# Optimization experiments

Hardware: AMD Instinct MI355X
Metric: run time of the kernel (lower is better)

The kernel has to match this reference:

```python
import jax, jax.numpy as jnp
import numpy as np

# Fixed query graph: 3 terms, 3 predicates, edges (head_term, tail_term, pred):
# (0,1,0), (1,2,1), (0,2,2) -> every term has degree 2 -> seq_len 3 incl. self.
T, P, B, D, H, NL, FF = 3, 3, 16384, 256, 8, 2, 1024
DH = D // H
SCALE = DH ** -0.5


def setup_inputs() -> dict:
    key = jax.random.key(0)
    ks = jax.random.split(key, 8)
    s = 0.02
    f = jnp.float32
    return {
        "term_embs": jax.random.normal(ks[0], (T, B, D), f),
        "pred_embs": jax.random.normal(ks[1], (P, B, D), f),
        "Wq": jax.random.normal(ks[2], (NL, D, D), f) * s,
        "Wk": jax.random.normal(ks[3], (NL, D, D), f) * s,
        "Wv": jax.random.normal(ks[4], (NL, D, D), f) * s,
        "Wo": jax.random.normal(ks[5], (NL, D, D), f) * s,
        "bq": jnp.zeros((NL, D), f),
        "bk": jnp.zeros((NL, D), f),
        "bv": jnp.zeros((NL, D), f),
        "bo": jnp.zeros((NL, D), f),
        "ln1_g": jnp.ones((NL, D), f),
        "ln1_b": jnp.zeros((NL, D), f),
        "ln2_g": jnp.ones((NL, D), f),
        "ln2_b": jnp.zeros((NL, D), f),
        "W1": jax.random.normal(ks[6], (NL, D, FF), f) * s,
        "b1": jnp.zeros((NL, FF), f),
        "W2": jax.random.normal(ks[7], (NL, FF, D), f) * s,
        "b2": jnp.zeros((NL, D), f),
        "lnf_g": jnp.ones((D,), f),
        "lnf_b": jnp.zeros((D,), f),
    }


def _layer_norm(x, g, b):
    m = jnp.mean(x, axis=-1, keepdims=True)
    v = jnp.var(x, axis=-1, keepdims=True)
    return (x - m) * jax.lax.rsqrt(v + 1e-5) * g + b


def _forward(term_embs, pred_embs, Wq, Wk, Wv, Wo, bq, bk, bv, bo,
             ln1_g, ln1_b, ln2_g, ln2_b, W1, b1, W2, b2, lnf_g, lnf_b):
    # --- message passing (TransE-style NBP): tail_est = head + pred, head_est = tail - pred
    # edge heads: [0,1,0], edge tails: [1,2,2]
    tail_msgs = term_embs[jnp.array([0, 1, 0])] + pred_embs  # [P,B,D] -> sent to tail terms
    head_msgs = term_embs[jnp.array([1, 2, 2])] - pred_embs  # [P,B,D] -> sent to head terms
    # collect per term (static gather) + self embedding appended last
    x0 = jnp.stack([head_msgs[0], head_msgs[2], term_embs[0]], axis=1)  # [B,3,D]
    x1 = jnp.stack([tail_msgs[0], head_msgs[1], term_embs[1]], axis=1)
    x2 = jnp.stack([tail_msgs[1], tail_msgs[2], term_embs[2]], axis=1)
    x = jnp.concatenate([x0, x1, x2], axis=0)  # [T*B, 3, D]
    # --- pre-norm Transformer encoder, NL layers (dropout off at eval)
    for l in range(NL):
        h = _layer_norm(x, ln1_g[l], ln1_b[l])
        q = (h @ Wq[l] + bq[l]).reshape(-1, 3, H, DH)
        k = (h @ Wk[l] + bk[l]).reshape(-1, 3, H, DH)
        v = (h @ Wv[l] + bv[l]).reshape(-1, 3, H, DH)
        a = jax.nn.softmax(jnp.einsum('nqhd,nkhd->nhqk', q, k) * SCALE, axis=-1)
        o = jnp.einsum('nhqk,nkhd->nqhd', a, v).reshape(-1, 3, D)
        x = x + o @ Wo[l] + bo[l]
        h = _layer_norm(x, ln2_g[l], ln2_b[l])
        x = x + jax.nn.relu(h @ W1[l] + b1[l]) @ W2[l] + b2[l]
    x = _layer_norm(x, lnf_g, lnf_b)
    # --- aggregate (agg_func='mean') over the small message sequence
    return jnp.mean(x, axis=1).reshape(T, B, D)


def reference(term_embs, pred_embs, Wq, Wk, Wv, Wo, bq, bk, bv, bo,
              ln1_g, ln1_b, ln2_g, ln2_b, W1, b1, W2, b2, lnf_g, lnf_b):
    return _forward(term_embs, pred_embs, Wq, Wk, Wv, Wo, bq, bk, bv, bo,
                    ln1_g, ln1_b, ln2_g, ln2_b, W1, b1, W2, b2, lnf_g, lnf_b)
```

## Files before the change

kernel.cpp:

```cpp
#include <hip/hip_runtime.h>
#include <hip/hip_bf16.h>
#include <stdint.h>

typedef __hip_bfloat16 bf16;
typedef unsigned short u16;
typedef unsigned int u32;
typedef __bf16 v8bf __attribute__((ext_vector_type(8)));
typedef float v4f __attribute__((ext_vector_type(4)));

#define NB 16384
#define MROWS 147456

__device__ __forceinline__ float b2f(u16 u) {
  union { u32 u; float f; } v; v.u = ((u32)u) << 16; return v.f;
}
__device__ __forceinline__ u16 f2b(float f) {
  union { float f; u32 u; } v; v.f = f;
  u32 u = v.u;
  return (u16)((u + 0x7fffu + ((u >> 16) & 1u)) >> 16);
}
__device__ __forceinline__ void async16(const u16* g, u16* lds) {
  __builtin_amdgcn_global_load_lds((const __attribute__((address_space(1))) void*)g,
                                   (__attribute__((address_space(3))) void*)lds,
                                   16, 0, 0);
}

__global__ __launch_bounds__(256)
void prep_weights(const float* Wq, const float* Wk, const float* Wv, const float* Wo,
                  const float* W1, const float* W2,
                  const float* bq, const float* bk, const float* bv,
                  bf16* wt, float* bqkv)
{
  if (blockIdx.x == 6144) {
    for (int e = threadIdx.x; e < 1536; e += 256) {
      int l = e / 768;
      int rem = e - l * 768;
      int wsel = rem >> 8;
      int col = rem & 255;
      const float* s = (wsel == 0) ? bq : (wsel == 1) ? bk : bv;
      bqkv[e] = s[l * 256 + col];
    }
    return;
  }
  int gid = blockIdx.x * 256 + threadIdx.x;
  int layer = (gid >= 786432) ? 1 : 0;
  int r = gid - layer * 786432;
  const float* src; int K, N, e, outoff;
  if (r < 262144) {
    int which = r >> 16;
    e = r & 65535; K = 256; N = 256;
    const float* w = (which == 0) ? Wq : (which == 1) ? Wk : (which == 2) ? Wv : Wo;
    src = w + layer * 65536;
    outoff = layer * 786432 + which * 65536;
  } else if (r < 524288) {
    e = r - 262144; K = 256; N = 1024;
    src = W1 + layer * 262144;
    outoff = layer * 786432 + 262144;
  } else {
    e = r - 524288; K = 1024; N = 256;
    src = W2 + layer * 262144;
    outoff = layer * 786432 + 524288;
  }
  int n = e / K, kk = e - n * K;
  ((u16*)wt)[outoff + e] = f2b(src[kk * N + n]);
}

__global__ __launch_bounds__(256)
void build_ln(const float* __restrict__ T, const float* __restrict__ P,
              const float* __restrict__ gp, const float* __restrict__ bp,
              float* __restrict__ X, bf16* __restrict__ H, int row0)
{
  const int lane = threadIdx.x & 63;
  const int lrow = blockIdx.x * 4 + (threadIdx.x >> 6);
  const int row = row0 + lrow;
  const int d0 = lane * 4;
  int n = row / 3;
  int t = row - n * 3;
  float4 v;
  if (t == 2) {
    v = *(const float4*)(T + (size_t)n * 256 + d0);
  } else {
    int tm = n >> 14, b = n & 16383;
    const int srcT[6] = {1, 2,  0, 2,  1, 0};
    const int srcP[6] = {0, 2,  0, 1,  1, 2};
    const float sg[6] = {-1.f, -1.f,  1.f, -1.f,  1.f, 1.f};
    int idx = tm * 2 + t;
    float4 tv = *(const float4*)(T + ((size_t)(srcT[idx] * NB + b)) * 256 + d0);
    float4 pv = *(const float4*)(P + ((size_t)(srcP[idx] * NB + b)) * 256 + d0);
    float s = sg[idx];
    v.x = tv.x + s * pv.x;
    v.y = tv.y + s * pv.y;
    v.z = tv.z + s * pv.z;
    v.w = tv.w + s * pv.w;
  }
  *(float4*)(X + (size_t)lrow * 256 + d0) = v;
  float s = v.x + v.y + v.z + v.w;
  float q = v.x * v.x + v.y * v.y + v.z * v.z + v.w * v.w;
  #pragma unroll
  for (int m = 32; m > 0; m >>= 1) {
    s += __shfl_xor(s, m, 64);
    q += __shfl_xor(q, m, 64);
  }
  float mean = s * (1.f / 256.f);
  float var = q * (1.f / 256.f) - mean * mean;
  float r = rsqrtf(var + 1e-5f);
  float4 gv = *(const float4*)(gp + d0);
  float4 bv = *(const float4*)(bp + d0);
  ushort4 outv;
  outv.x = f2b((v.x - mean) * r * gv.x + bv.x);
  outv.y = f2b((v.y - mean) * r * gv.y + bv.y);
  outv.z = f2b((v.z - mean) * r * gv.z + bv.z);
  outv.w = f2b((v.w - mean) * r * gv.w + bv.w);
  *(ushort4*)((u16*)H + (size_t)lrow * 256 + d0) = outv;
}

__global__ __launch_bounds__(256)
void ln_rows(const float* __restrict__ xp, const float* __restrict__ gp,
             const float* __restrict__ bp, bf16* __restrict__ hp)
{
  const int lane = threadIdx.x & 63;
  const int row = blockIdx.x * 4 + (threadIdx.x >> 6);
  float4 rv = *(const float4*)(xp + (size_t)row * 256 + lane * 4);
  float v0 = rv.x, v1 = rv.y, v2 = rv.z, v3 = rv.w;
  float s = v0 + v1 + v2 + v3;
  float q = v0 * v0 + v1 * v1 + v2 * v2 + v3 * v3;
  #pragma unroll
  for (int m = 32; m > 0; m >>= 1) {
    s += __shfl_xor(s, m, 64);
    q += __shfl_xor(q, m, 64);
  }
  float mean = s * (1.f / 256.f);
  float var = q * (1.f / 256.f) - mean * mean;
  float r = rsqrtf(var + 1e-5f);
  float4 gv = *(const float4*)(gp + lane * 4);
  float4 bv = *(const float4*)(bp + lane * 4);
  ushort4 outv;
  outv.x = f2b((v0 - mean) * r * gv.x + bv.x);
  outv.y = f2b((v1 - mean) * r * gv.y + bv.y);
  outv.z = f2b((v2 - mean) * r * gv.z + bv.z);
  outv.w = f2b((v3 - mean) * r * gv.w + bv.w);
  *(ushort4*)((u16*)hp + (size_t)row * 256 + lane * 4) = outv;
}

template<int RES, int RELU, int OUTF32>
__global__ __launch_bounds__(256)
void gemm_bt(const bf16* __restrict__ Ap, const bf16* __restrict__ Btp,
             const float* __restrict__ biasp, const float* __restrict__ resp,
             void* __restrict__ Cp, int N, int K,
             int btZ, int biasZ, long long cZ)
{
  __shared__ __align__(16) u16 As[2 * 128 * 32];
  __shared__ __align__(16) u16 Bs[2 * 128 * 32];
  const int z = blockIdx.z;
  const u16* A = (const u16*)Ap;
  const u16* Bt = (const u16*)Btp + (size_t)z * btZ;
  const float* bias = biasp + (size_t)z * biasZ;
  const int m0 = blockIdx.x * 128;
  const int n0 = blockIdx.y * 128;
  const int tid = threadIdx.x;
  const int w = tid >> 6, lane = tid & 63;
  const int waveM = (w & 1) * 64, waveN = (w >> 1) * 64;

  const int rrow = tid >> 2;
  const int kcol = (tid & 3) * 8;
  const u16* pA0 = A + (size_t)(m0 + rrow) * K + kcol;
  const u16* pA1 = A + (size_t)(m0 + rrow + 64) * K + kcol;
  const u16* pB0 = Bt + (size_t)(n0 + rrow) * K + kcol;
  const u16* pB1 = Bt + (size_t)(n0 + rrow + 64) * K + kcol;

  v4f acc[4][4];
  #pragma unroll
  for (int i = 0; i < 4; i++)
    #pragma unroll
    for (int j = 0; j < 4; j++) {
      v4f zz = {0.f, 0.f, 0.f, 0.f};
      acc[i][j] = zz;
    }

  const int rdA = (waveM + (lane & 15)) * 64 + (lane >> 4) * 16;
  const int rdB = (waveN + (lane & 15)) * 64 + (lane >> 4) * 16;
  const int nk = K >> 5;

  async16(pA0, As + w * 512);        async16(pA1, As + 2048 + w * 512);
  async16(pB0, Bs + w * 512);        async16(pB1, Bs + 2048 + w * 512);
  pA0 += 32; pA1 += 32; pB0 += 32; pB1 += 32;

  int cur = 0;
  for (int kt = 0; kt < nk; kt++) {
    __syncthreads();
    if (kt + 1 < nk) {
      const int nxt = (cur ^ 1) * 4096;
      async16(pA0, As + nxt + w * 512);        async16(pA1, As + nxt + 2048 + w * 512);
      async16(pB0, Bs + nxt + w * 512);        async16(pB1, Bs + nxt + 2048 + w * 512);
      pA0 += 32; pA1 += 32; pB0 += 32; pB1 += 32;
    }
    const char* AsC = (const char*)(As + cur * 4096);
    const char* BsC = (const char*)(Bs + cur * 4096);
    v8bf a[4], b[4];
    #pragma unroll
    for (int i = 0; i < 4; i++)
      a[i] = *(const v8bf*)(AsC + rdA + i * 1024);
    #pragma unroll
    for (int j = 0; j < 4; j++)
      b[j] = *(const v8bf*)(BsC + rdB + j * 1024);
    #pragma unroll
    for (int i = 0; i < 4; i++)
      #pragma unroll
      for (int j = 0; j < 4; j++)
        acc[i][j] = __builtin_amdgcn_mfma_f32_16x16x32_bf16(a[i], b[j], acc[i][j], 0, 0, 0);
    cur ^= 1;
  }

  float bv[4];
  #pragma unroll
  for (int j = 0; j < 4; j++)
    bv[j] = bias[n0 + waveN + j * 16 + (lane & 15)];

  #pragma unroll
  for (int i = 0; i < 4; i++) {
    #pragma unroll
    for (int r = 0; r < 4; r++) {
      int rowg = m0 + waveM + i * 16 + (lane >> 4) * 4 + r;
      size_t rb = (size_t)rowg * N;
      #pragma unroll
      for (int j = 0; j < 4; j++) {
        int colg = n0 + waveN + j * 16 + (lane & 15);
        float vv = acc[i][j][r] + bv[j];
        if (RES) vv += resp[rb + colg];
        if (RELU) vv = fmaxf(vv, 0.f);
        if (OUTF32) ((float*)Cp)[rb + colg] = vv;
        else ((u16*)Cp + (size_t)z * cZ)[rb + colg] = f2b(vv);
      }
    }
  }
}

__global__ __launch_bounds__(256)
void attn(const bf16* __restrict__ qp, const bf16* __restrict__ kp,
          const bf16* __restrict__ vp, bf16* __restrict__ op)
{
  __shared__ __align__(16) u16 qs[6144], ks[6144], vs[6144];
  __shared__ float probs[8][8][9];
  const int tid = threadIdx.x;
  const size_t gbase = (size_t)blockIdx.x * 6144;
  const uint4* qg = (const uint4*)((const u16*)qp + gbase);
  const uint4* kg = (const uint4*)((const u16*)kp + gbase);
  const uint4* vg = (const uint4*)((const u16*)vp + gbase);
  for (int c = tid; c < 768; c += 256) {
    ((uint4*)qs)[c] = qg[c];
    ((uint4*)ks)[c] = kg[c];
    ((uint4*)vs)[c] = vg[c];
  }
  __syncthreads();
  if (tid < 64) {
    int s = tid >> 3, h = tid & 7;
    int base = s * 768 + h * 32;
    float sc[3][3];
    #pragma unroll
    for (int i = 0; i < 3; i++)
      #pragma unroll
      for (int j = 0; j < 3; j++) {
        float sum = 0.f;
        #pragma unroll
        for (int d = 0; d < 32; d++)
          sum += b2f(qs[base + i * 256 + d]) * b2f(ks[base + j * 256 + d]);
        sc[i][j] = sum * 0.17677669529663687f;
      }
    #pragma unroll
    for (int i = 0; i < 3; i++) {
      float m = fmaxf(sc[i][0], fmaxf(sc[i][1], sc[i][2]));
      float e0 = __expf(sc[i][0] - m);
      float e1 = __expf(sc[i][1] - m);
      float e2 = __expf(sc[i][2] - m);
      float inv = 1.f / (e0 + e1 + e2);
      probs[s][h][i * 3 + 0] = e0 * inv;
      probs[s][h][i * 3 + 1] = e1 * inv;
      probs[s][h][i * 3 + 2] = e2 * inv;
    }
  }
  __syncthreads();
  u16* og = (u16*)op + gbase;
  for (int c = tid; c < 6144; c += 256) {
    int lrow = c >> 8, hd = c & 255;
    int s = lrow / 3, i = lrow - s * 3;
    int h = hd >> 5;
    float p0 = probs[s][h][i * 3 + 0];
    float p1 = probs[s][h][i * 3 + 1];
    float p2 = probs[s][h][i * 3 + 2];
    float o = p0 * b2f(vs[s * 768 + hd])
            + p1 * b2f(vs[s * 768 + 256 + hd])
            + p2 * b2f(vs[s * 768 + 512 + hd]);
    og[c] = f2b(o);
  }
}

__global__ __launch_bounds__(256)
void ln_final_mean(const float* __restrict__ xp, const float* __restrict__ gp,
                   const float* __restrict__ bp, float* __restrict__ outp)
{
  const int lane = threadIdx.x & 63;
  const int n = blockIdx.x * 4 + (threadIdx.x >> 6);
  float4 gv = *(const float4*)(gp + lane * 4);
  float4 bv4 = *(const float4*)(bp + lane * 4);
  float a0 = 0.f, a1 = 0.f, a2 = 0.f, a3 = 0.f;
  for (int t = 0; t < 3; t++) {
    float4 rv = *(const float4*)(xp + ((size_t)n * 3 + t) * 256 + lane * 4);
    float v0 = rv.x, v1 = rv.y, v2 = rv.z, v3 = rv.w;
    float s = v0 + v1 + v2 + v3;
    float q = v0 * v0 + v1 * v1 + v2 * v2 + v3 * v3;
    #pragma unroll
    for (int m = 32; m > 0; m >>= 1) {
      s += __shfl_xor(s, m, 64);
      q += __shfl_xor(q, m, 64);
    }
    float mean = s * (1.f / 256.f);
    float var = q * (1.f / 256.f) - mean * mean;
    float r = rsqrtf(var + 1e-5f);
    a0 += (v0 - mean) * r * gv.x + bv4.x;
    a1 += (v1 - mean) * r * gv.y + bv4.y;
    a2 += (v2 - mean) * r * gv.z + bv4.z;
    a3 += (v3 - mean) * r * gv.w + bv4.w;
  }
  const float third = 1.f / 3.f;
  float4 outv;
  outv.x = a0 * third;
  outv.y = a1 * third;
  outv.z = a2 * third;
  outv.w = a3 * third;
  *(float4*)(outp + (size_t)n * 256 + lane * 4) = outv;
}

extern "C" void kernel_launch(void* const* d_in, const int* in_sizes, int n_in,
                              void* d_out, int out_size, void* d_ws, size_t ws_size,
                              hipStream_t stream)
{
  const float* term = (const float*)d_in[0];
  const float* pred = (const float*)d_in[1];
  const float* Wq  = (const float*)d_in[2];
  const float* Wk  = (const float*)d_in[3];
  const float* Wv  = (const float*)d_in[4];
  const float* Wo  = (const float*)d_in[5];
  const float* bq  = (const float*)d_in[6];
  const float* bk  = (const float*)d_in[7];
  const float* bvv = (const float*)d_in[8];
  const float* bo  = (const float*)d_in[9];
  const float* ln1g = (const float*)d_in[10];
  const float* ln1b = (const float*)d_in[11];
  const float* ln2g = (const float*)d_in[12];
  const float* ln2b = (const float*)d_in[13];
  const float* W1  = (const float*)d_in[14];
  const float* b1  = (const float*)d_in[15];
  const float* W2  = (const float*)d_in[16];
  const float* b2  = (const float*)d_in[17];
  const float* lnfg = (const float*)d_in[18];
  const float* lnfb = (const float*)d_in[19];

  int nch = 128;
  for (int c = 1; c <= 128; c *= 2) {
    size_t Mc = (size_t)MROWS / c;
    size_t need = 4ull * 1024 * 1024 + Mc * 3584ull;
    if (need <= ws_size) { nch = c; break; }
  }
  const size_t Mc = (size_t)MROWS / nch;
  const int mBlocks = (int)(Mc / 128);

  char* ws = (char*)d_ws;
  bf16* wt   = (bf16*)ws;
  float* bqkv = (float*)(ws + 3145728);
  float* x = (float*)(ws + 4194304);
  bf16* h = (bf16*)(x + Mc * 256);
  bf16* q = h + Mc * 256;
  bf16* v_ = q + 2 * Mc * 256;
  bf16* o = q + 3 * Mc * 256;
  bf16* f = q;

  prep_weights<<<6145, 256, 0, stream>>>(Wq, Wk, Wv, Wo, W1, W2, bq, bk, bvv, wt, bqkv);

  const long long qkvZ = (long long)(Mc * 256);
  for (int ch = 0; ch < nch; ch++) {
    const int row0 = (int)(ch * Mc);
    build_ln<<<(int)(Mc / 4), 256, 0, stream>>>(term, pred, ln1g, ln1b, x, h, row0);
    for (int l = 0; l < 2; l++) {
      const bf16* wl = wt + l * 786432;
      if (l > 0)
        ln_rows<<<(int)(Mc / 4), 256, 0, stream>>>(x, ln1g + l * 256, ln1b + l * 256, h);
      gemm_bt<0, 0, 0><<<dim3(mBlocks, 2, 3), 256, 0, stream>>>(
          h, wl, bqkv + l * 768, nullptr, q, 256, 256, 65536, 256, qkvZ);
      attn<<<(int)(Mc / 24), 256, 0, stream>>>(q, q + Mc * 256, v_, o);
      gemm_bt<1, 0, 1><<<dim3(mBlocks, 2, 1), 256, 0, stream>>>(
          o, wl + 196608, bo + l * 256, x, x, 256, 256, 0, 0, 0);
      ln_rows<<<(int)(Mc / 4), 256, 0, stream>>>(x, ln2g + l * 256, ln2b + l * 256, h);
      gemm_bt<0, 1, 0><<<dim3(mBlocks, 8, 1), 256, 0, stream>>>(
          h, wl + 262144, b1 + l * 1024, nullptr, f, 1024, 256, 0, 0, 0);
      gemm_bt<1, 0, 1><<<dim3(mBlocks, 2, 1), 256, 0, stream>>>(
          f, wl + 524288, b2 + l * 256, x, x, 256, 1024, 0, 0, 0);
    }
    ln_final_mean<<<(int)(Mc / 12), 256, 0, stream>>>(
        x, lnfg, lnfb, (float*)d_out + (size_t)(row0 / 3) * 256);
  }
}
```

Before: 1.592 ms.

## Register-prefetch GEMM pipeline and fuse QKV into one interleaved GEMM output

The GEMM drops the global_load_lds async copies. It now stages tiles through registers with a two-deep prefetch: it loads tiles kt+3 and kt+4 into registers while computing on LDS double buffers, unrolled by two. The Q, K and V projections become a single N=768 GEMM writing an interleaved row layout, and the attention kernel reads strided q/k/v slices from it. This is meant to hide global latency better and remove the z-dimension indexing. The cost is more register pressure, and the layout relies on the weights being packed contiguously as a 768x256 block.

```diff
diff --git a/kernel.cpp b/kernel.cpp
--- a/kernel.cpp
+++ b/kernel.cpp
@@ -18,11 +18,6 @@
   union { float f; u32 u; } v; v.f = f;
   u32 u = v.u;
   return (u16)((u + 0x7fffu + ((u >> 16) & 1u)) >> 16);
-}
-__device__ __forceinline__ void async16(const u16* g, u16* lds) {
-  __builtin_amdgcn_global_load_lds((const __attribute__((address_space(1))) void*)g,
-                                   (__attribute__((address_space(3))) void*)lds,
-                                   16, 0, 0);
 }
 
 __global__ __launch_bounds__(256)
@@ -142,19 +137,49 @@
   *(ushort4*)((u16*)hp + (size_t)row * 256 + lane * 4) = outv;
 }
 
+#define LDT(dst, t) do {                                            \
+    int tt = (t) < nk ? (t) : nk - 1;                               \
+    dst[0] = *(const uint4*)(pA0 + tt * 32);                        \
+    dst[1] = *(const uint4*)(pA1 + tt * 32);                        \
+    dst[2] = *(const uint4*)(pB0 + tt * 32);                        \
+    dst[3] = *(const uint4*)(pB1 + tt * 32);                        \
+  } while (0)
+
+#define WRT(src, buf) do {                                          \
+    ((uint4*)As)[(buf) * 512 + tid] = src[0];                       \
+    ((uint4*)As)[(buf) * 512 + 256 + tid] = src[1];                 \
+    ((uint4*)Bs)[(buf) * 512 + tid] = src[2];                       \
+    ((uint4*)Bs)[(buf) * 512 + 256 + tid] = src[3];                 \
+  } while (0)
+
+#define CMPT(buf) do {                                              \
+    const char* AsC = (const char*)As + (buf) * 8192;               \
+    const char* BsC = (const char*)Bs + (buf) * 8192;               \
+    v8bf a[4], b[4];                                                \
+    _Pragma("unroll")                                               \
+    for (int i = 0; i < 4; i++)                                     \
+      a[i] = *(const v8bf*)(AsC + rdA + i * 1024);                  \
+    _Pragma("unroll")                                               \
+    for (int j = 0; j < 4; j++)                                     \
+      b[j] = *(const v8bf*)(BsC + rdB + j * 1024);                  \
+    _Pragma("unroll")                                               \
+    for (int i = 0; i < 4; i++)                                     \
+      _Pragma("unroll")                                             \
+      for (int j = 0; j < 4; j++)                                   \
+        acc[i][j] = __builtin_amdgcn_mfma_f32_16x16x32_bf16(        \
+            a[i], b[j], acc[i][j], 0, 0, 0);                        \
+  } while (0)
+
 template<int RES, int RELU, int OUTF32>
 __global__ __launch_bounds__(256)
 void gemm_bt(const bf16* __restrict__ Ap, const bf16* __restrict__ Btp,
              const float* __restrict__ biasp, const float* __restrict__ resp,
-             void* __restrict__ Cp, int N, int K,
-             int btZ, int biasZ, long long cZ)
+             void* __restrict__ Cp, int N, int K)
 {
   __shared__ __align__(16) u16 As[2 * 128 * 32];
   __shared__ __align__(16) u16 Bs[2 * 128 * 32];
-  const int z = blockIdx.z;
   const u16* A = (const u16*)Ap;
-  const u16* Bt = (const u16*)Btp + (size_t)z * btZ;
-  const float* bias = biasp + (size_t)z * biasZ;
+  const u16* Bt = (const u16*)Btp;
   const int m0 = blockIdx.x * 128;
   const int n0 = blockIdx.y * 128;
   const int tid = threadIdx.x;
@@ -164,9 +189,10 @@
   const int rrow = tid >> 2;
   const int kcol = (tid & 3) * 8;
   const u16* pA0 = A + (size_t)(m0 + rrow) * K + kcol;
-  const u16* pA1 = A + (size_t)(m0 + rrow + 64) * K + kcol;
+  const u16* pA1 = pA0 + (size_t)64 * K;
   const u16* pB0 = Bt + (size_t)(n0 + rrow) * K + kcol;
-  const u16* pB1 = Bt + (size_t)(n0 + rrow + 64) * K + kcol;
+  const u16* pB1 = pB0 + (size_t)64 * K;
+  const int nk = K >> 5;
 
   v4f acc[4][4];
   #pragma unroll
@@ -179,42 +205,29 @@
 
   const int rdA = (waveM + (lane & 15)) * 64 + (lane >> 4) * 16;
   const int rdB = (waveN + (lane & 15)) * 64 + (lane >> 4) * 16;
-  const int nk = K >> 5;
-
-  async16(pA0, As + w * 512);        async16(pA1, As + 2048 + w * 512);
-  async16(pB0, Bs + w * 512);        async16(pB1, Bs + 2048 + w * 512);
-  pA0 += 32; pA1 += 32; pB0 += 32; pB1 += 32;
-
-  int cur = 0;
-  for (int kt = 0; kt < nk; kt++) {
+
+  uint4 R[4], S[4];
+  LDT(R, 0);
+  LDT(S, 1);
+  WRT(R, 0);
+  LDT(R, 2);
+  __syncthreads();
+
+  for (int kt = 0; kt < nk; kt += 2) {
+    WRT(S, 1);
+    LDT(S, kt + 3);
+    CMPT(0);
     __syncthreads();
-    if (kt + 1 < nk) {
-      const int nxt = (cur ^ 1) * 4096;
-      async16(pA0, As + nxt + w * 512);        async16(pA1, As + nxt + 2048 + w * 512);
-      async16(pB0, Bs + nxt + w * 512);        async16(pB1, Bs + nxt + 2048 + w * 512);
-      pA0 += 32; pA1 += 32; pB0 += 32; pB1 += 32;
-    }
-    const char* AsC = (const char*)(As + cur * 4096);
-    const char* BsC = (const char*)(Bs + cur * 4096);
-    v8bf a[4], b[4];
-    #pragma unroll
-    for (int i = 0; i < 4; i++)
-      a[i] = *(const v8bf*)(AsC + rdA + i * 1024);
-    #pragma unroll
-    for (int j = 0; j < 4; j++)
-      b[j] = *(const v8bf*)(BsC + rdB + j * 1024);
-    #pragma unroll
-    for (int i = 0; i < 4; i++)
-      #pragma unroll
-      for (int j = 0; j < 4; j++)
-        acc[i][j] = __builtin_amdgcn_mfma_f32_16x16x32_bf16(a[i], b[j], acc[i][j], 0, 0, 0);
-    cur ^= 1;
+    WRT(R, 0);
+    LDT(R, kt + 4);
+    CMPT(1);
+    __syncthreads();
   }
 
   float bv[4];
   #pragma unroll
   for (int j = 0; j < 4; j++)
-    bv[j] = bias[n0 + waveN + j * 16 + (lane & 15)];
+    bv[j] = biasp[n0 + waveN + j * 16 + (lane & 15)];
 
   #pragma unroll
   for (int i = 0; i < 4; i++) {
@@ -229,27 +242,24 @@
         if (RES) vv += resp[rb + colg];
         if (RELU) vv = fmaxf(vv, 0.f);
         if (OUTF32) ((float*)Cp)[rb + colg] = vv;
-        else ((u16*)Cp + (size_t)z * cZ)[rb + colg] = f2b(vv);
+        else ((u16*)Cp)[rb + colg] = f2b(vv);
       }
     }
   }
 }
 
 __global__ __launch_bounds__(256)
-void attn(const bf16* __restrict__ qp, const bf16* __restrict__ kp,
-          const bf16* __restrict__ vp, bf16* __restrict__ op)
+void attn(const bf16* __restrict__ qkvp, bf16* __restrict__ op)
 {
   __shared__ __align__(16) u16 qs[6144], ks[6144], vs[6144];
   __shared__ float probs[8][8][9];
   const int tid = threadIdx.x;
-  const size_t gbase = (size_t)blockIdx.x * 6144;
-  const uint4* qg = (const uint4*)((const u16*)qp + gbase);
-  const uint4* kg = (const uint4*)((const u16*)kp + gbase);
-  const uint4* vg = (const uint4*)((const u16*)vp + gbase);
+  const uint4* g = (const uint4*)qkvp + (size_t)blockIdx.x * 24 * 96;
   for (int c = tid; c < 768; c += 256) {
-    ((uint4*)qs)[c] = qg[c];
-    ((uint4*)ks)[c] = kg[c];
-    ((uint4*)vs)[c] = vg[c];
+    int r = c >> 5, e = c & 31;
+    ((uint4*)qs)[c] = g[r * 96 + e];
+    ((uint4*)ks)[c] = g[r * 96 + 32 + e];
+    ((uint4*)vs)[c] = g[r * 96 + 64 + e];
   }
   __syncthreads();
   if (tid < 64) {
@@ -279,7 +289,7 @@
     }
   }
   __syncthreads();
-  u16* og = (u16*)op + gbase;
+  u16* og = (u16*)op + (size_t)blockIdx.x * 6144;
   for (int c = tid; c < 6144; c += 256) {
     int lrow = c >> 8, hd = c & 255;
     int s = lrow / 3, i = lrow - s * 3;
@@ -369,14 +379,12 @@
   float* bqkv = (float*)(ws + 3145728);
   float* x = (float*)(ws + 4194304);
   bf16* h = (bf16*)(x + Mc * 256);
-  bf16* q = h + Mc * 256;
-  bf16* v_ = q + 2 * Mc * 256;
-  bf16* o = q + 3 * Mc * 256;
-  bf16* f = q;
+  bf16* qkv = h + Mc * 256;
+  bf16* o = qkv + Mc * 768;
+  bf16* f = qkv;
 
   prep_weights<<<6145, 256, 0, stream>>>(Wq, Wk, Wv, Wo, W1, W2, bq, bk, bvv, wt, bqkv);
 
-  const long long qkvZ = (long long)(Mc * 256);
   for (int ch = 0; ch < nch; ch++) {
     const int row0 = (int)(ch * Mc);
     build_ln<<<(int)(Mc / 4), 256, 0, stream>>>(term, pred, ln1g, ln1b, x, h, row0);
@@ -384,16 +392,16 @@
       const bf16* wl = wt + l * 786432;
       if (l > 0)
         ln_rows<<<(int)(Mc / 4), 256, 0, stream>>>(x, ln1g + l * 256, ln1b + l * 256, h);
-      gemm_bt<0, 0, 0><<<dim3(mBlocks, 2, 3), 256, 0, stream>>>(
-          h, wl, bqkv + l * 768, nullptr, q, 256, 256, 65536, 256, qkvZ);
-      attn<<<(int)(Mc / 24), 256, 0, stream>>>(q, q + Mc * 256, v_, o);
-      gemm_bt<1, 0, 1><<<dim3(mBlocks, 2, 1), 256, 0, stream>>>(
-          o, wl + 196608, bo + l * 256, x, x, 256, 256, 0, 0, 0);
+      gemm_bt<0, 0, 0><<<dim3(mBlocks, 6), 256, 0, stream>>>(
+          h, wl, bqkv + l * 768, nullptr, qkv, 768, 256);
+      attn<<<(int)(Mc / 24), 256, 0, stream>>>(qkv, o);
+      gemm_bt<1, 0, 1><<<dim3(mBlocks, 2), 256, 0, stream>>>(
+          o, wl + 196608, bo + l * 256, x, x, 256, 256);
       ln_rows<<<(int)(Mc / 4), 256, 0, stream>>>(x, ln2g + l * 256, ln2b + l * 256, h);
-      gemm_bt<0, 1, 0><<<dim3(mBlocks, 8, 1), 256, 0, stream>>>(
-          h, wl + 262144, b1 + l * 1024, nullptr, f, 1024, 256, 0, 0, 0);
-      gemm_bt<1, 0, 1><<<dim3(mBlocks, 2, 1), 256, 0, stream>>>(
-          f, wl + 524288, b2 + l * 256, x, x, 256, 1024, 0, 0, 0);
+      gemm_bt<0, 1, 0><<<dim3(mBlocks, 8), 256, 0, stream>>>(
+          h, wl + 262144, b1 + l * 1024, nullptr, f, 1024, 256);
+      gemm_bt<1, 0, 1><<<dim3(mBlocks, 2), 256, 0, stream>>>(
+          f, wl + 524288, b2 + l * 256, x, x, 256, 1024);
     }
     ln_final_mean<<<(int)(Mc / 12), 256, 0, stream>>>(
         x, lnfg, lnfb, (float*)d_out + (size_t)(row0 / 3) * 256);
```

Result: slower. 3.832 ms (+140.8%).

## Fuse LN2 and FFN into one kernel and pack QKV into one GEMM

Applied to the files above, without the earlier changes.

Adds an ffn_fused kernel that computes LayerNorm2, the W1 GEMM with ReLU, and the W2 GEMM with residual for a 32-row tile. The 32x1024 intermediate stays in LDS, so the bf16 FFN activation is never written to or read from global memory. The QKV projection becomes a single N=768 GEMM writing an interleaved qkv buffer, and attn is adjusted to read that layout. The cost is weight operands loaded straight from global/cache without LDS staging, plus 80KB of LDS per block, which limits occupancy.

```diff
diff --git a/kernel.cpp b/kernel.cpp
--- a/kernel.cpp
+++ b/kernel.cpp
@@ -142,19 +142,16 @@
   *(ushort4*)((u16*)hp + (size_t)row * 256 + lane * 4) = outv;
 }
 
-template<int RES, int RELU, int OUTF32>
+template<int RES, int OUTF32>
 __global__ __launch_bounds__(256)
 void gemm_bt(const bf16* __restrict__ Ap, const bf16* __restrict__ Btp,
              const float* __restrict__ biasp, const float* __restrict__ resp,
-             void* __restrict__ Cp, int N, int K,
-             int btZ, int biasZ, long long cZ)
+             void* __restrict__ Cp, int N, int K)
 {
   __shared__ __align__(16) u16 As[2 * 128 * 32];
   __shared__ __align__(16) u16 Bs[2 * 128 * 32];
-  const int z = blockIdx.z;
   const u16* A = (const u16*)Ap;
-  const u16* Bt = (const u16*)Btp + (size_t)z * btZ;
-  const float* bias = biasp + (size_t)z * biasZ;
+  const u16* Bt = (const u16*)Btp;
   const int m0 = blockIdx.x * 128;
   const int n0 = blockIdx.y * 128;
   const int tid = threadIdx.x;
@@ -164,9 +161,9 @@
   const int rrow = tid >> 2;
   const int kcol = (tid & 3) * 8;
   const u16* pA0 = A + (size_t)(m0 + rrow) * K + kcol;
-  const u16* pA1 = A + (size_t)(m0 + rrow + 64) * K + kcol;
+  const u16* pA1 = pA0 + (size_t)64 * K;
   const u16* pB0 = Bt + (size_t)(n0 + rrow) * K + kcol;
-  const u16* pB1 = Bt + (size_t)(n0 + rrow + 64) * K + kcol;
+  const u16* pB1 = pB0 + (size_t)64 * K;
 
   v4f acc[4][4];
   #pragma unroll
@@ -214,7 +211,7 @@
   float bv[4];
   #pragma unroll
   for (int j = 0; j < 4; j++)
-    bv[j] = bias[n0 + waveN + j * 16 + (lane & 15)];
+    bv[j] = biasp[n0 + waveN + j * 16 + (lane & 15)];
 
   #pragma unroll
   for (int i = 0; i < 4; i++) {
@@ -227,29 +224,147 @@
         int colg = n0 + waveN + j * 16 + (lane & 15);
         float vv = acc[i][j][r] + bv[j];
         if (RES) vv += resp[rb + colg];
-        if (RELU) vv = fmaxf(vv, 0.f);
         if (OUTF32) ((float*)Cp)[rb + colg] = vv;
-        else ((u16*)Cp + (size_t)z * cZ)[rb + colg] = f2b(vv);
+        else ((u16*)Cp)[rb + colg] = f2b(vv);
       }
     }
   }
 }
 
 __global__ __launch_bounds__(256)
-void attn(const bf16* __restrict__ qp, const bf16* __restrict__ kp,
-          const bf16* __restrict__ vp, bf16* __restrict__ op)
+void ffn_fused(float* __restrict__ xp,
+               const bf16* __restrict__ W1Tp, const bf16* __restrict__ W2Tp,
+               const float* __restrict__ gp, const float* __restrict__ bp,
+               const float* __restrict__ b1p, const float* __restrict__ b2p)
+{
+  __shared__ __align__(16) u16 hs[8 * 1024];
+  __shared__ __align__(16) u16 fs[32 * 1024];
+  const int tid = threadIdx.x;
+  const int w = tid >> 6, lane = tid & 63;
+  const int ln15 = lane & 15, lq = lane >> 4;
+  const int r0 = blockIdx.x * 32;
+  const u16* W1T = (const u16*)W1Tp;
+  const u16* W2T = (const u16*)W2Tp;
+
+  #pragma unroll
+  for (int rr = 0; rr < 8; rr++) {
+    int row = rr * 4 + w;
+    int d0 = lane * 4;
+    float4 v = *(const float4*)(xp + (size_t)(r0 + row) * 256 + d0);
+    float s = v.x + v.y + v.z + v.w;
+    float q = v.x * v.x + v.y * v.y + v.z * v.z + v.w * v.w;
+    #pragma unroll
+    for (int m = 32; m > 0; m >>= 1) {
+      s += __shfl_xor(s, m, 64);
+      q += __shfl_xor(q, m, 64);
+    }
+    float mean = s * (1.f / 256.f);
+    float var = q * (1.f / 256.f) - mean * mean;
+    float r = rsqrtf(var + 1e-5f);
+    float4 gv = *(const float4*)(gp + d0);
+    float4 bv = *(const float4*)(bp + d0);
+    ushort4 o4;
+    o4.x = f2b((v.x - mean) * r * gv.x + bv.x);
+    o4.y = f2b((v.y - mean) * r * gv.y + bv.y);
+    o4.z = f2b((v.z - mean) * r * gv.z + bv.z);
+    o4.w = f2b((v.w - mean) * r * gv.w + bv.w);
+    *(ushort4*)(hs + (d0 >> 5) * 1024 + row * 32 + (d0 & 31)) = o4;
+  }
+  __syncthreads();
+
+  #pragma unroll 1
+  for (int p = 0; p < 4; p++) {
+    const int nb = w * 256 + p * 64;
+    v4f acc[2][4];
+    #pragma unroll
+    for (int i = 0; i < 2; i++)
+      #pragma unroll
+      for (int j = 0; j < 4; j++) {
+        v4f zz = {0.f, 0.f, 0.f, 0.f};
+        acc[i][j] = zz;
+      }
+    #pragma unroll
+    for (int kk = 0; kk < 8; kk++) {
+      v8bf a[2], b[4];
+      #pragma unroll
+      for (int i = 0; i < 2; i++)
+        a[i] = *(const v8bf*)(hs + kk * 1024 + (ln15 + 16 * i) * 32 + lq * 8);
+      #pragma unroll
+      for (int j = 0; j < 4; j++)
+        b[j] = *(const v8bf*)(W1T + (size_t)(nb + 16 * j + ln15) * 256 + kk * 32 + lq * 8);
+      #pragma unroll
+      for (int i = 0; i < 2; i++)
+        #pragma unroll
+        for (int j = 0; j < 4; j++)
+          acc[i][j] = __builtin_amdgcn_mfma_f32_16x16x32_bf16(a[i], b[j], acc[i][j], 0, 0, 0);
+    }
+    #pragma unroll
+    for (int j = 0; j < 4; j++) {
+      int col = nb + 16 * j + ln15;
+      float bb = b1p[col];
+      int tbase = (col >> 5) * 1024 + (col & 31);
+      #pragma unroll
+      for (int i = 0; i < 2; i++)
+        #pragma unroll
+        for (int r = 0; r < 4; r++) {
+          int row = 16 * i + lq * 4 + r;
+          fs[tbase + row * 32] = f2b(fmaxf(acc[i][j][r] + bb, 0.f));
+        }
+    }
+  }
+  __syncthreads();
+
+  const int cb = w * 64;
+  v4f acc2[2][4];
+  #pragma unroll
+  for (int i = 0; i < 2; i++)
+    #pragma unroll
+    for (int j = 0; j < 4; j++) {
+      v4f zz = {0.f, 0.f, 0.f, 0.f};
+      acc2[i][j] = zz;
+    }
+  #pragma unroll 4
+  for (int kk = 0; kk < 32; kk++) {
+    v8bf a[2], b[4];
+    #pragma unroll
+    for (int i = 0; i < 2; i++)
+      a[i] = *(const v8bf*)(fs + kk * 1024 + (ln15 + 16 * i) * 32 + lq * 8);
+    #pragma unroll
+    for (int j = 0; j < 4; j++)
+      b[j] = *(const v8bf*)(W2T + (size_t)(cb + 16 * j + ln15) * 1024 + kk * 32 + lq * 8);
+    #pragma unroll
+    for (int i = 0; i < 2; i++)
+      #pragma unroll
+      for (int j = 0; j < 4; j++)
+        acc2[i][j] = __builtin_amdgcn_mfma_f32_16x16x32_bf16(a[i], b[j], acc2[i][j], 0, 0, 0);
+  }
+  #pragma unroll
+  for (int j = 0; j < 4; j++) {
+    int colg = cb + 16 * j + ln15;
+    float bb = b2p[colg];
+    #pragma unroll
+    for (int i = 0; i < 2; i++)
+      #pragma unroll
+      for (int r = 0; r < 4; r++) {
+        int rowg = r0 + 16 * i + lq * 4 + r;
+        size_t idx = (size_t)rowg * 256 + colg;
+        xp[idx] += acc2[i][j][r] + bb;
+      }
+  }
+}
+
+__global__ __launch_bounds__(256)
+void attn(const bf16* __restrict__ qkvp, bf16* __restrict__ op)
 {
   __shared__ __align__(16) u16 qs[6144], ks[6144], vs[6144];
   __shared__ float probs[8][8][9];
   const int tid = threadIdx.x;
-  const size_t gbase = (size_t)blockIdx.x * 6144;
-  const uint4* qg = (const uint4*)((const u16*)qp + gbase);
-  const uint4* kg = (const uint4*)((const u16*)kp + gbase);
-  const uint4* vg = (const uint4*)((const u16*)vp + gbase);
+  const uint4* g = (const uint4*)qkvp + (size_t)blockIdx.x * 24 * 96;
   for (int c = tid; c < 768; c += 256) {
-    ((uint4*)qs)[c] = qg[c];
-    ((uint4*)ks)[c] = kg[c];
-    ((uint4*)vs)[c] = vg[c];
+    int r = c >> 5, e = c & 31;
+    ((uint4*)qs)[c] = g[r * 96 + e];
+    ((uint4*)ks)[c] = g[r * 96 + 32 + e];
+    ((uint4*)vs)[c] = g[r * 96 + 64 + e];
   }
   __syncthreads();
   if (tid < 64) {
@@ -279,7 +394,7 @@
     }
   }
   __syncthreads();
-  u16* og = (u16*)op + gbase;
+  u16* og = (u16*)op + (size_t)blockIdx.x * 6144;
   for (int c = tid; c < 6144; c += 256) {
     int lrow = c >> 8, hd = c & 255;
     int s = lrow / 3, i = lrow - s * 3;
@@ -369,14 +484,11 @@
   float* bqkv = (float*)(ws + 3145728);
   float* x = (float*)(ws + 4194304);
   bf16* h = (bf16*)(x + Mc * 256);
-  bf16* q = h + Mc * 256;
-  bf16* v_ = q + 2 * Mc * 256;
-  bf16* o = q + 3 * Mc * 256;
-  bf16* f = q;
+  bf16* qkv = h + Mc * 256;
+  bf16* o = qkv + Mc * 768;
 
   prep_weights<<<6145, 256, 0, stream>>>(Wq, Wk, Wv, Wo, W1, W2, bq, bk, bvv, wt, bqkv);
 
-  const long long qkvZ = (long long)(Mc * 256);
   for (int ch = 0; ch < nch; ch++) {
     const int row0 = (int)(ch * Mc);
     build_ln<<<(int)(Mc / 4), 256, 0, stream>>>(term, pred, ln1g, ln1b, x, h, row0);
@@ -384,16 +496,14 @@
       const bf16* wl = wt + l * 786432;
       if (l > 0)
         ln_rows<<<(int)(Mc / 4), 256, 0, stream>>>(x, ln1g + l * 256, ln1b + l * 256, h);
-      gemm_bt<0, 0, 0><<<dim3(mBlocks, 2, 3), 256, 0, stream>>>(
-          h, wl, bqkv + l * 768, nullptr, q, 256, 256, 65536, 256, qkvZ);
-      attn<<<(int)(Mc / 24), 256, 0, stream>>>(q, q + Mc * 256, v_, o);
-      gemm_bt<1, 0, 1><<<dim3(mBlocks, 2, 1), 256, 0, stream>>>(
-          o, wl + 196608, bo + l * 256, x, x, 256, 256, 0, 0, 0);
-      ln_rows<<<(int)(Mc / 4), 256, 0, stream>>>(x, ln2g + l * 256, ln2b + l * 256, h);
-      gemm_bt<0, 1, 0><<<dim3(mBlocks, 8, 1), 256, 0, stream>>>(
-          h, wl + 262144, b1 + l * 1024, nullptr, f, 1024, 256, 0, 0, 0);
-      gemm_bt<1, 0, 1><<<dim3(mBlocks, 2, 1), 256, 0, stream>>>(
-          f, wl + 524288, b2 + l * 256, x, x, 256, 1024, 0, 0, 0);
+      gemm_bt<0, 0><<<dim3(mBlocks, 6), 256, 0, stream>>>(
+          h, wl, bqkv + l * 768, nullptr, qkv, 768, 256);
+      attn<<<(int)(Mc / 24), 256, 0, stream>>>(qkv, o);
+      gemm_bt<1, 1><<<dim3(mBlocks, 2), 256, 0, stream>>>(
+          o, wl + 196608, bo + l * 256, x, x, 256, 256);
+      ffn_fused<<<(int)(Mc / 32), 256, 0, stream>>>(
+          x, (const bf16*)(wl + 262144), (const bf16*)(wl + 524288),
+          ln2g + l * 256, ln2b + l * 256, b1 + l * 1024, b2 + l * 256);
     }
     ln_final_mean<<<(int)(Mc / 12), 256, 0, stream>>>(
         x, lnfg, lnfb, (float*)d_out + (size_t)(row0 / 3) * 256);
```

New measurement: 2.024 ms. 1.27x slower.
